# Kernel tuning notes

Measured on AMD Instinct MI355X. Metric: run time of the kernel, lower is better.

The kernel has to match this reference:

```python
import jax, jax.numpy as jnp
import numpy as np

DIM = 768
N_HEADS = 12
HEAD_DIM = DIM // N_HEADS
SCALE = HEAD_DIM ** -0.5


def setup_inputs() -> dict:
    key = jax.random.key(0)
    k_x, k_qkv, k_proj, k_pb = jax.random.split(key, 4)
    B, N = 8, 1024
    x = jax.random.normal(k_x, (B, N, DIM), dtype=jnp.float32)
    # torch nn.Linear weight layout: [out_features, in_features], y = x @ W.T
    w_qkv = jax.random.normal(k_qkv, (3 * DIM, DIM), dtype=jnp.float32) * (DIM ** -0.5)
    w_proj = jax.random.normal(k_proj, (DIM, DIM), dtype=jnp.float32) * (DIM ** -0.5)
    b_proj = jax.random.normal(k_pb, (DIM,), dtype=jnp.float32) * 0.01
    # init_mode='quadratic': alpha=0.125, beta=0.5, gamma=0.0, shape [H,1,1]
    alpha = jnp.full((N_HEADS, 1, 1), 0.125, dtype=jnp.float32)
    beta = jnp.full((N_HEADS, 1, 1), 0.5, dtype=jnp.float32)
    gamma = jnp.zeros((N_HEADS, 1, 1), dtype=jnp.float32)
    return {"x": x, "w_qkv": w_qkv, "w_proj": w_proj, "b_proj": b_proj,
            "alpha": alpha, "beta": beta, "gamma": gamma}


def reference(x, w_qkv, w_proj, b_proj, alpha, beta, gamma):
    B, N, C = x.shape
    qkv = x @ w_qkv.T  # [B, N, 3C]
    qkv = qkv.reshape(B, N, 3, N_HEADS, HEAD_DIM)
    qkv = jnp.transpose(qkv, (2, 0, 3, 1, 4))  # [3, B, H, N, d]
    q, k, v = qkv[0], qkv[1], qkv[2]
    logits = jnp.einsum('bhnd,bhmd->bhnm', q, k) * SCALE  # [B, H, N, N]
    a = alpha[None]  # broadcast over batch: [1, H, 1, 1]
    b = beta[None]
    g = gamma[None]
    attn = jax.nn.relu(a * logits * logits + b * logits + g)
    attn = attn / (jnp.sum(attn, axis=-1, keepdims=True) + 1e-6)
    out = jnp.einsum('bhnm,bhmd->bhnd', attn, v)  # [B, H, N, d]
    out = jnp.transpose(out, (0, 2, 1, 3)).reshape(B, N, C)
    return out @ w_proj.T + b_proj
```

## Files before the change

kernel.cpp:

```cpp
#include <hip/hip_runtime.h>


typedef _Float16 f16x8 __attribute__((ext_vector_type(8)));
typedef _Float16 f16x4 __attribute__((ext_vector_type(4)));
typedef float f32x4 __attribute__((ext_vector_type(4)));

#define NB 8
#define NN 1024
#define NC 768
#define NH 12
#define ND 64
#define TC 2304
#define NM 8192

__device__ __forceinline__ void async16(const void* g, void* l) {
    __builtin_amdgcn_global_load_lds(
        (const __attribute__((address_space(1))) void*)g,
        (__attribute__((address_space(3))) void*)l, 16, 0, 0);
}

__global__ void cvt_f32_f16(const float* __restrict__ s, _Float16* __restrict__ d, int n4) {
    int i = blockIdx.x * 256 + threadIdx.x;
    if (i < n4) {
        float4 v = ((const float4*)s)[i];
        f16x4 o;
        o[0] = (_Float16)v.x; o[1] = (_Float16)v.y;
        o[2] = (_Float16)v.z; o[3] = (_Float16)v.w;
        ((f16x4*)d)[i] = o;
    }
}

__global__ void cvt_split_f32(const float* __restrict__ s, _Float16* __restrict__ hi,
                              _Float16* __restrict__ lo, int n4) {
    int i = blockIdx.x * 256 + threadIdx.x;
    if (i < n4) {
        float4 v = ((const float4*)s)[i];
        f16x4 h, l;
        h[0] = (_Float16)v.x; l[0] = (_Float16)(v.x - (float)h[0]);
        h[1] = (_Float16)v.y; l[1] = (_Float16)(v.y - (float)h[1]);
        h[2] = (_Float16)v.z; l[2] = (_Float16)(v.z - (float)h[2]);
        h[3] = (_Float16)v.w; l[3] = (_Float16)(v.w - (float)h[3]);
        ((f16x4*)hi)[i] = h;
        ((f16x4*)lo)[i] = l;
    }
}

__global__ __launch_bounds__(256) void gemm_qkv(
    const _Float16* __restrict__ Ah, const _Float16* __restrict__ Bh,
    _Float16* __restrict__ q16, _Float16* __restrict__ k16,
    _Float16* __restrict__ vt16)
{
    __shared__ __align__(16) _Float16 sAh[128 * 32];
    __shared__ __align__(16) _Float16 sBh[128 * 32];
    const int tid = threadIdx.x;
    const int lane = tid & 63, wv = tid >> 6;
    const int quad = lane >> 4, l16 = lane & 15;
    const int wm = (wv >> 1) * 64, wn = (wv & 1) * 64;
    const int m0 = blockIdx.x * 128, n0 = blockIdx.y * 128;

    f32x4 acc[4][4] = {};

    for (int k0 = 0; k0 < NC; k0 += 32) {
#pragma unroll
        for (int i = 0; i < 2; i++) {
            int c = tid + i * 256;
            int r = c >> 2, kc = c & 3;
            async16(Ah + (size_t)(m0 + r) * NC + k0 + kc * 8, sAh + c * 8);
            async16(Bh + (size_t)(n0 + r) * NC + k0 + kc * 8, sBh + c * 8);
        }
        __syncthreads();
        f16x8 ah[4], bh[4];
#pragma unroll
        for (int t = 0; t < 4; t++) {
            ah[t] = *(const f16x8*)(sAh + (wm + t * 16 + l16) * 32 + quad * 8);
            bh[t] = *(const f16x8*)(sBh + (wn + t * 16 + l16) * 32 + quad * 8);
        }
#pragma unroll
        for (int i = 0; i < 4; i++)
#pragma unroll
            for (int j = 0; j < 4; j++)
                acc[i][j] = __builtin_amdgcn_mfma_f32_16x16x32_f16(ah[i], bh[j], acc[i][j], 0, 0, 0);
        __syncthreads();
    }

    const int col = n0 + wn + l16;
#pragma unroll
    for (int j = 0; j < 4; j++) {
        int cj = col + j * 16;
        int which = cj / NC;
        int w2 = cj - which * NC;
        int h = w2 >> 6, dd = w2 & 63;
#pragma unroll
        for (int i = 0; i < 4; i++) {
            int row = m0 + wm + i * 16 + quad * 4;
            int b = row >> 10, nr = row & 1023;
            int bhd = b * NH + h;
            if (which == 2) {
                f16x4 v4;
                v4[0] = (_Float16)acc[i][j][0];
                v4[1] = (_Float16)acc[i][j][1];
                v4[2] = (_Float16)acc[i][j][2];
                v4[3] = (_Float16)acc[i][j][3];
                *(f16x4*)(vt16 + ((size_t)(bhd * ND + dd)) * NN + nr) = v4;
            } else {
                _Float16* dst = (which == 0 ? q16 : k16);
#pragma unroll
                for (int r = 0; r < 4; r++)
                    dst[((size_t)(bhd * NN + nr + r)) * ND + dd] = (_Float16)acc[i][j][r];
            }
        }
    }
}

__global__ __launch_bounds__(256) void attn_kernel(
    const _Float16* __restrict__ q16, const _Float16* __restrict__ k16,
    const _Float16* __restrict__ vt16, float* __restrict__ outh32,
    const float* __restrict__ alpha, const float* __restrict__ beta,
    const float* __restrict__ gamma)
{
    const int qt = blockIdx.x, bh = blockIdx.y;
    const int b = bh / NH, h = bh - b * NH;
    const int tid = threadIdx.x, lane = tid & 63, wv = tid >> 6;
    const int quad = lane >> 4, l16 = lane & 15;
    const float a2 = alpha[h] * 0.015625f;
    const float b1 = beta[h] * 0.125f;
    const float g0 = gamma[h];

    __shared__ __align__(16) _Float16 sKh[128 * 64];
    __shared__ __align__(16) _Float16 sVt[64 * 128];

    const _Float16* Qb = q16 + ((size_t)(bh * NN + qt * 128)) * ND;
    const _Float16* Kb = k16 + (size_t)bh * NN * ND;
    const _Float16* Vb = vt16 + (size_t)bh * ND * NN;

    f16x8 qf[2][2];
#pragma unroll
    for (int mt = 0; mt < 2; mt++)
#pragma unroll
        for (int ksd = 0; ksd < 2; ksd++)
            qf[mt][ksd] = *(const f16x8*)(Qb + (size_t)(wv * 32 + mt * 16 + l16) * ND
                                          + ksd * 32 + quad * 8);

    f32x4 O[4][2] = {};
    float dsum[2] = {0.f, 0.f};

    for (int kt = 0; kt < 8; kt++) {
#pragma unroll
        for (int i = 0; i < 4; i++) {
            int P = tid + i * 256;
            int f = P >> 6, q = (P >> 4) & 3, a = (P >> 2) & 3, bb = P & 3;
            int ks2 = f >> 2, T = (f >> 1) & 1, ksd = f & 1;
            int row = ks2 * 32 + 8 * a + 4 * T + bb;
            async16(Kb + (size_t)(kt * 128 + row) * ND + (ksd * 4 + q) * 8, sKh + P * 8);
        }
#pragma unroll
        for (int i = 0; i < 4; i++) {
            int P = tid + i * 256;
            int f = P >> 6, q = (P >> 4) & 3, l = P & 15;
            int ks2 = f >> 2, dt = f & 3;
            async16(Vb + (size_t)(dt * 16 + l) * NN + kt * 128 + (ks2 * 4 + q) * 8,
                    sVt + P * 8);
        }
        __syncthreads();

        f16x8 bfrag[2][4];
#pragma unroll
        for (int T = 0; T < 2; T++) {
            f32x4 S[2][4] = {};
#pragma unroll
            for (int ks2 = 0; ks2 < 4; ks2++) {
#pragma unroll
                for (int ksd = 0; ksd < 2; ksd++) {
                    int addr = (((ks2 * 4 + T * 2 + ksd) * 64) + quad * 16 + l16) * 8;
                    f16x8 ah = *(const f16x8*)(sKh + addr);
#pragma unroll
                    for (int mt = 0; mt < 2; mt++)
                        S[mt][ks2] = __builtin_amdgcn_mfma_f32_16x16x32_f16(ah, qf[mt][ksd], S[mt][ks2], 0, 0, 0);
                }
            }
#pragma unroll
            for (int mt = 0; mt < 2; mt++) {
#pragma unroll
                for (int ks2 = 0; ks2 < 4; ks2++) {
#pragma unroll
                    for (int r = 0; r < 4; r++) {
                        float s = S[mt][ks2][r];
                        float w = fmaxf(fmaf(fmaf(a2, s, b1), s, g0), 0.f);
                        _Float16 wh = (_Float16)w;
                        dsum[mt] += (float)wh;
                        bfrag[mt][ks2][(T << 2) | r] = wh;
                    }
                }
            }
        }

#pragma unroll
        for (int ks2 = 0; ks2 < 4; ks2++) {
#pragma unroll
            for (int dt = 0; dt < 4; dt++) {
                int addr = (((ks2 * 4 + dt) * 64) + quad * 16 + l16) * 8;
                f16x8 vf = *(const f16x8*)(sVt + addr);
#pragma unroll
                for (int mt = 0; mt < 2; mt++)
                    O[dt][mt] = __builtin_amdgcn_mfma_f32_16x16x32_f16(vf, bfrag[mt][ks2], O[dt][mt], 0, 0, 0);
            }
        }
        __syncthreads();
    }

    float rinv[2];
#pragma unroll
    for (int mt = 0; mt < 2; mt++) {
        float v = dsum[mt];
        v += __shfl_xor(v, 16);
        v += __shfl_xor(v, 32);
        rinv[mt] = 1.0f / (v + 1e-6f);
    }

    const int base_row = qt * 128 + wv * 32;
#pragma unroll
    for (int dt = 0; dt < 4; dt++) {
#pragma unroll
        for (int mt = 0; mt < 2; mt++) {
            float4 o4;
            o4.x = O[dt][mt][0] * rinv[mt];
            o4.y = O[dt][mt][1] * rinv[mt];
            o4.z = O[dt][mt][2] * rinv[mt];
            o4.w = O[dt][mt][3] * rinv[mt];
            int row = base_row + mt * 16 + l16;
            int col = h * ND + dt * 16 + quad * 4;
            *(float4*)(outh32 + (size_t)(b * NN + row) * NC + col) = o4;
        }
    }
}

__global__ __launch_bounds__(256) void gemm_proj(
    const float* __restrict__ A,
    const _Float16* __restrict__ Bh, const _Float16* __restrict__ Bl,
    const float* __restrict__ bias, float* __restrict__ out)
{
    __shared__ __align__(16) _Float16 sAh[128 * 32];
    __shared__ __align__(16) _Float16 sAl[128 * 32];
    __shared__ __align__(16) _Float16 sBh[64 * 32];
    __shared__ __align__(16) _Float16 sBl[64 * 32];
    const int tid = threadIdx.x;
    const int lane = tid & 63, wv = tid >> 6;
    const int quad = lane >> 4, l16 = lane & 15;
    const int wm = (wv >> 1) * 64, wn = (wv & 1) * 32;
    const int m0 = blockIdx.x * 128, n0 = blockIdx.y * 64;

    f32x4 acc[4][2] = {};

    for (int k0 = 0; k0 < NC; k0 += 32) {
#pragma unroll
        for (int i = 0; i < 2; i++) {
            int c = tid + i * 256;
            int r = c >> 2, kc = c & 3;
            const float4* pa = (const float4*)(A + (size_t)(m0 + r) * NC + k0 + kc * 8);
            float4 v0 = pa[0], v1 = pa[1];
            f16x8 hi8, lo8;
            hi8[0] = (_Float16)v0.x; lo8[0] = (_Float16)(v0.x - (float)hi8[0]);
            hi8[1] = (_Float16)v0.y; lo8[1] = (_Float16)(v0.y - (float)hi8[1]);
            hi8[2] = (_Float16)v0.z; lo8[2] = (_Float16)(v0.z - (float)hi8[2]);
            hi8[3] = (_Float16)v0.w; lo8[3] = (_Float16)(v0.w - (float)hi8[3]);
            hi8[4] = (_Float16)v1.x; lo8[4] = (_Float16)(v1.x - (float)hi8[4]);
            hi8[5] = (_Float16)v1.y; lo8[5] = (_Float16)(v1.y - (float)hi8[5]);
            hi8[6] = (_Float16)v1.z; lo8[6] = (_Float16)(v1.z - (float)hi8[6]);
            hi8[7] = (_Float16)v1.w; lo8[7] = (_Float16)(v1.w - (float)hi8[7]);
            *(f16x8*)(sAh + c * 8) = hi8;
            *(f16x8*)(sAl + c * 8) = lo8;
        }
        {
            int r = tid >> 2, kc = tid & 3;
            size_t goB = (size_t)(n0 + r) * NC + k0 + kc * 8;
            async16(Bh + goB, sBh + tid * 8);
            async16(Bl + goB, sBl + tid * 8);
        }
        __syncthreads();
        f16x8 ah[4], al[4], bh[2], bl[2];
#pragma unroll
        for (int t = 0; t < 4; t++) {
            ah[t] = *(const f16x8*)(sAh + (wm + t * 16 + l16) * 32 + quad * 8);
            al[t] = *(const f16x8*)(sAl + (wm + t * 16 + l16) * 32 + quad * 8);
        }
#pragma unroll
        for (int t = 0; t < 2; t++) {
            bh[t] = *(const f16x8*)(sBh + (wn + t * 16 + l16) * 32 + quad * 8);
            bl[t] = *(const f16x8*)(sBl + (wn + t * 16 + l16) * 32 + quad * 8);
        }
#pragma unroll
        for (int i = 0; i < 4; i++)
#pragma unroll
            for (int j = 0; j < 2; j++)
                acc[i][j] = __builtin_amdgcn_mfma_f32_16x16x32_f16(ah[i], bh[j], acc[i][j], 0, 0, 0);
#pragma unroll
        for (int i = 0; i < 4; i++)
#pragma unroll
            for (int j = 0; j < 2; j++)
                acc[i][j] = __builtin_amdgcn_mfma_f32_16x16x32_f16(al[i], bh[j], acc[i][j], 0, 0, 0);
#pragma unroll
        for (int i = 0; i < 4; i++)
#pragma unroll
            for (int j = 0; j < 2; j++)
                acc[i][j] = __builtin_amdgcn_mfma_f32_16x16x32_f16(ah[i], bl[j], acc[i][j], 0, 0, 0);
        __syncthreads();
    }

#pragma unroll
    for (int i = 0; i < 4; i++) {
#pragma unroll
        for (int j = 0; j < 2; j++) {
#pragma unroll
            for (int r = 0; r < 4; r++) {
                int row = m0 + wm + i * 16 + quad * 4 + r;
                int col = n0 + wn + j * 16 + l16;
                out[(size_t)row * NC + col] = acc[i][j][r] + bias[col];
            }
        }
    }
}

extern "C" void kernel_launch(void* const* d_in, const int* in_sizes, int n_in,
                              void* d_out, int out_size, void* d_ws, size_t ws_size,
                              hipStream_t stream) {
    const float* x      = (const float*)d_in[0];
    const float* w_qkv  = (const float*)d_in[1];
    const float* w_proj = (const float*)d_in[2];
    const float* b_proj = (const float*)d_in[3];
    const float* alpha  = (const float*)d_in[4];
    const float* beta   = (const float*)d_in[5];
    const float* gamma  = (const float*)d_in[6];
    float* out = (float*)d_out;

    char* ws = (char*)d_ws;
    float*    outh32 = (float*)(ws + 0);
    _Float16* xh     = (_Float16*)(ws + 25165824);
    _Float16* wqkvh  = (_Float16*)(ws + 37748736);
    _Float16* wprojh = (_Float16*)(ws + 41287680);
    _Float16* wprojl = (_Float16*)(ws + 42467328);
    _Float16* q16    = (_Float16*)(ws + 43646976);
    _Float16* k16    = (_Float16*)(ws + 56229888);
    _Float16* vt16   = (_Float16*)(ws + 68812800);

    cvt_f32_f16<<<6144, 256, 0, stream>>>(x, xh, 1572864);
    cvt_f32_f16<<<1728, 256, 0, stream>>>(w_qkv, wqkvh, 442368);
    cvt_split_f32<<<576, 256, 0, stream>>>(w_proj, wprojh, wprojl, 147456);

    gemm_qkv<<<dim3(64, 18), 256, 0, stream>>>(xh, wqkvh, q16, k16, vt16);
    attn_kernel<<<dim3(8, 96), 256, 0, stream>>>(q16, k16, vt16, outh32, alpha, beta, gamma);
    gemm_proj<<<dim3(64, 12), 256, 0, stream>>>(outh32, wprojh, wprojl, b_proj, out);
}
```

Measured before the change: 215.6 us.

## Widen GEMM K-tiles, swizzle LDS layout, stage epilogue stores, pre-split attention output

Both GEMMs now load 64-wide K tiles into a fragment-ordered LDS layout, so each lane's MFMA operand reads are contiguous and conflict-free. Each tile therefore needs half as many barrier round trips. The QKV epilogue stages results through shared memory and writes Q/K rows and V-transpose rows with 16-byte vector stores instead of scattered scalar stores. The attention kernel now writes its output as fp16 hi/lo pairs, so gemm_proj can load A asynchronously instead of converting fp32 in the load loop. The cost is more LDS per block, which may lower occupancy.

```diff
diff --git a/kernel.cpp b/kernel.cpp
--- a/kernel.cpp
+++ b/kernel.cpp
@@ -46,75 +46,99 @@
 }
 
 __global__ __launch_bounds__(256) void gemm_qkv(
-    const _Float16* __restrict__ Ah, const _Float16* __restrict__ Bh,
+    const _Float16* __restrict__ Ah, const _Float16* __restrict__ Bw,
     _Float16* __restrict__ q16, _Float16* __restrict__ k16,
     _Float16* __restrict__ vt16)
 {
-    __shared__ __align__(16) _Float16 sAh[128 * 32];
-    __shared__ __align__(16) _Float16 sBh[128 * 32];
+    __shared__ __align__(16) _Float16 sm[2 * 128 * 64];
+    _Float16* sA = sm;
+    _Float16* sB = sm + 128 * 64;
     const int tid = threadIdx.x;
     const int lane = tid & 63, wv = tid >> 6;
     const int quad = lane >> 4, l16 = lane & 15;
-    const int wm = (wv >> 1) * 64, wn = (wv & 1) * 64;
+    const int wmh = wv >> 1, wnh = wv & 1;
+    const int wm = wmh * 64, wn = wnh * 64;
     const int m0 = blockIdx.x * 128, n0 = blockIdx.y * 128;
 
     f32x4 acc[4][4] = {};
 
-    for (int k0 = 0; k0 < NC; k0 += 32) {
-#pragma unroll
-        for (int i = 0; i < 2; i++) {
-            int c = tid + i * 256;
-            int r = c >> 2, kc = c & 3;
-            async16(Ah + (size_t)(m0 + r) * NC + k0 + kc * 8, sAh + c * 8);
-            async16(Bh + (size_t)(n0 + r) * NC + k0 + kc * 8, sBh + c * 8);
-        }
-        __syncthreads();
-        f16x8 ah[4], bh[4];
-#pragma unroll
-        for (int t = 0; t < 4; t++) {
-            ah[t] = *(const f16x8*)(sAh + (wm + t * 16 + l16) * 32 + quad * 8);
-            bh[t] = *(const f16x8*)(sBh + (wn + t * 16 + l16) * 32 + quad * 8);
-        }
+    for (int k0 = 0; k0 < NC; k0 += 64) {
+#pragma unroll
+        for (int i = 0; i < 4; i++) {
+            int P = tid + i * 256;
+            int f = P >> 6, q = (P >> 4) & 3, l = P & 15;
+            int half = f >> 3, t = (f >> 1) & 3, ksd = f & 1;
+            int row = half * 64 + t * 16 + l;
+            int ch = ksd * 4 + q;
+            async16(Ah + (size_t)(m0 + row) * NC + k0 + ch * 8, sA + P * 8);
+            async16(Bw + (size_t)(n0 + row) * NC + k0 + ch * 8, sB + P * 8);
+        }
+        __syncthreads();
+#pragma unroll
+        for (int ksd = 0; ksd < 2; ksd++) {
+            f16x8 a4[4], b4[4];
+#pragma unroll
+            for (int t = 0; t < 4; t++) {
+                a4[t] = *(const f16x8*)(sA + (((wmh * 4 + t) * 2 + ksd) * 64 + quad * 16 + l16) * 8);
+                b4[t] = *(const f16x8*)(sB + (((wnh * 4 + t) * 2 + ksd) * 64 + quad * 16 + l16) * 8);
+            }
+#pragma unroll
+            for (int i = 0; i < 4; i++)
+#pragma unroll
+                for (int j = 0; j < 4; j++)
+                    acc[i][j] = __builtin_amdgcn_mfma_f32_16x16x32_f16(a4[i], b4[j], acc[i][j], 0, 0, 0);
+        }
+        __syncthreads();
+    }
+
+    _Float16* sT = sm;
+    const bool is_v = (n0 >= 2 * NC);
+    if (!is_v) {
 #pragma unroll
         for (int i = 0; i < 4; i++)
 #pragma unroll
             for (int j = 0; j < 4; j++)
-                acc[i][j] = __builtin_amdgcn_mfma_f32_16x16x32_f16(ah[i], bh[j], acc[i][j], 0, 0, 0);
-        __syncthreads();
-    }
-
-    const int col = n0 + wn + l16;
-#pragma unroll
-    for (int j = 0; j < 4; j++) {
-        int cj = col + j * 16;
-        int which = cj / NC;
-        int w2 = cj - which * NC;
-        int h = w2 >> 6, dd = w2 & 63;
-#pragma unroll
-        for (int i = 0; i < 4; i++) {
-            int row = m0 + wm + i * 16 + quad * 4;
-            int b = row >> 10, nr = row & 1023;
-            int bhd = b * NH + h;
-            if (which == 2) {
+#pragma unroll
+                for (int r = 0; r < 4; r++)
+                    sT[(wm + i * 16 + quad * 4 + r) * 128 + wn + j * 16 + l16] =
+                        (_Float16)acc[i][j][r];
+        __syncthreads();
+        int row = tid >> 1, hh = tid & 1;
+        int grow = m0 + row, b = grow >> 10, nr = grow & 1023;
+        int gc = n0 + hh * 64;
+        int which = gc / NC, w2 = gc - which * NC, h = w2 >> 6;
+        _Float16* dst = which ? k16 : q16;
+        size_t base = ((size_t)((b * NH + h) * NN + nr)) * ND;
+#pragma unroll
+        for (int c = 0; c < 8; c++)
+            *(f16x8*)(dst + base + c * 8) = *(const f16x8*)(sT + row * 128 + hh * 64 + c * 8);
+    } else {
+#pragma unroll
+        for (int i = 0; i < 4; i++)
+#pragma unroll
+            for (int j = 0; j < 4; j++) {
                 f16x4 v4;
                 v4[0] = (_Float16)acc[i][j][0];
                 v4[1] = (_Float16)acc[i][j][1];
                 v4[2] = (_Float16)acc[i][j][2];
                 v4[3] = (_Float16)acc[i][j][3];
-                *(f16x4*)(vt16 + ((size_t)(bhd * ND + dd)) * NN + nr) = v4;
-            } else {
-                _Float16* dst = (which == 0 ? q16 : k16);
-#pragma unroll
-                for (int r = 0; r < 4; r++)
-                    dst[((size_t)(bhd * NN + nr + r)) * ND + dd] = (_Float16)acc[i][j][r];
-            }
-        }
+                *(f16x4*)(sT + (wn + j * 16 + l16) * 128 + wm + i * 16 + quad * 4) = v4;
+            }
+        __syncthreads();
+        int ch = tid >> 1, th = tid & 1;
+        int w2 = n0 - 2 * NC + ch, h = w2 >> 6, dd = w2 & 63;
+        int b = m0 >> 10, nr0 = (m0 & 1023) + th * 64;
+        size_t base = ((size_t)((b * NH + h) * ND + dd)) * NN + nr0;
+#pragma unroll
+        for (int c = 0; c < 8; c++)
+            *(f16x8*)(vt16 + base + c * 8) = *(const f16x8*)(sT + ch * 128 + th * 64 + c * 8);
     }
 }
 
 __global__ __launch_bounds__(256) void attn_kernel(
     const _Float16* __restrict__ q16, const _Float16* __restrict__ k16,
-    const _Float16* __restrict__ vt16, float* __restrict__ outh32,
+    const _Float16* __restrict__ vt16,
+    _Float16* __restrict__ ohA, _Float16* __restrict__ olA,
     const float* __restrict__ alpha, const float* __restrict__ beta,
     const float* __restrict__ gamma)
 {
@@ -222,87 +246,96 @@
     for (int dt = 0; dt < 4; dt++) {
 #pragma unroll
         for (int mt = 0; mt < 2; mt++) {
-            float4 o4;
-            o4.x = O[dt][mt][0] * rinv[mt];
-            o4.y = O[dt][mt][1] * rinv[mt];
-            o4.z = O[dt][mt][2] * rinv[mt];
-            o4.w = O[dt][mt][3] * rinv[mt];
+            f16x4 h4, l4;
+#pragma unroll
+            for (int r = 0; r < 4; r++) {
+                float v = O[dt][mt][r] * rinv[mt];
+                _Float16 hv = (_Float16)v;
+                h4[r] = hv;
+                l4[r] = (_Float16)(v - (float)hv);
+            }
             int row = base_row + mt * 16 + l16;
             int col = h * ND + dt * 16 + quad * 4;
-            *(float4*)(outh32 + (size_t)(b * NN + row) * NC + col) = o4;
+            size_t addr = (size_t)(b * NN + row) * NC + col;
+            *(f16x4*)(ohA + addr) = h4;
+            *(f16x4*)(olA + addr) = l4;
         }
     }
 }
 
 __global__ __launch_bounds__(256) void gemm_proj(
-    const float* __restrict__ A,
+    const _Float16* __restrict__ Ah, const _Float16* __restrict__ Al,
     const _Float16* __restrict__ Bh, const _Float16* __restrict__ Bl,
     const float* __restrict__ bias, float* __restrict__ out)
 {
-    __shared__ __align__(16) _Float16 sAh[128 * 32];
-    __shared__ __align__(16) _Float16 sAl[128 * 32];
-    __shared__ __align__(16) _Float16 sBh[64 * 32];
-    __shared__ __align__(16) _Float16 sBl[64 * 32];
+    __shared__ __align__(16) _Float16 sAh[128 * 64];
+    __shared__ __align__(16) _Float16 sAl[128 * 64];
+    __shared__ __align__(16) _Float16 sBh[64 * 64];
+    __shared__ __align__(16) _Float16 sBl[64 * 64];
     const int tid = threadIdx.x;
     const int lane = tid & 63, wv = tid >> 6;
     const int quad = lane >> 4, l16 = lane & 15;
-    const int wm = (wv >> 1) * 64, wn = (wv & 1) * 32;
+    const int wmh = wv >> 1, wnh = wv & 1;
+    const int wm = wmh * 64, wn = wnh * 32;
     const int m0 = blockIdx.x * 128, n0 = blockIdx.y * 64;
 
     f32x4 acc[4][2] = {};
 
-    for (int k0 = 0; k0 < NC; k0 += 32) {
+    for (int k0 = 0; k0 < NC; k0 += 64) {
+#pragma unroll
+        for (int i = 0; i < 4; i++) {
+            int P = tid + i * 256;
+            int f = P >> 6, q = (P >> 4) & 3, l = P & 15;
+            int half = f >> 3, t = (f >> 1) & 3, ksd = f & 1;
+            int row = half * 64 + t * 16 + l;
+            int ch = ksd * 4 + q;
+            size_t src = (size_t)(m0 + row) * NC + k0 + ch * 8;
+            async16(Ah + src, sAh + P * 8);
+            async16(Al + src, sAl + P * 8);
+        }
 #pragma unroll
         for (int i = 0; i < 2; i++) {
-            int c = tid + i * 256;
-            int r = c >> 2, kc = c & 3;
-            const float4* pa = (const float4*)(A + (size_t)(m0 + r) * NC + k0 + kc * 8);
-            float4 v0 = pa[0], v1 = pa[1];
-            f16x8 hi8, lo8;
-            hi8[0] = (_Float16)v0.x; lo8[0] = (_Float16)(v0.x - (float)hi8[0]);
-            hi8[1] = (_Float16)v0.y; lo8[1] = (_Float16)(v0.y - (float)hi8[1]);
-            hi8[2] = (_Float16)v0.z; lo8[2] = (_Float16)(v0.z - (float)hi8[2]);
-            hi8[3] = (_Float16)v0.w; lo8[3] = (_Float16)(v0.w - (float)hi8[3]);
-            hi8[4] = (_Float16)v1.x; lo8[4] = (_Float16)(v1.x - (float)hi8[4]);
-            hi8[5] = (_Float16)v1.y; lo8[5] = (_Float16)(v1.y - (float)hi8[5]);
-            hi8[6] = (_Float16)v1.z; lo8[6] = (_Float16)(v1.z - (float)hi8[6]);
-            hi8[7] = (_Float16)v1.w; lo8[7] = (_Float16)(v1.w - (float)hi8[7]);
-            *(f16x8*)(sAh + c * 8) = hi8;
-            *(f16x8*)(sAl + c * 8) = lo8;
-        }
-        {
-            int r = tid >> 2, kc = tid & 3;
-            size_t goB = (size_t)(n0 + r) * NC + k0 + kc * 8;
-            async16(Bh + goB, sBh + tid * 8);
-            async16(Bl + goB, sBl + tid * 8);
-        }
-        __syncthreads();
-        f16x8 ah[4], al[4], bh[2], bl[2];
-#pragma unroll
-        for (int t = 0; t < 4; t++) {
-            ah[t] = *(const f16x8*)(sAh + (wm + t * 16 + l16) * 32 + quad * 8);
-            al[t] = *(const f16x8*)(sAl + (wm + t * 16 + l16) * 32 + quad * 8);
-        }
-#pragma unroll
-        for (int t = 0; t < 2; t++) {
-            bh[t] = *(const f16x8*)(sBh + (wn + t * 16 + l16) * 32 + quad * 8);
-            bl[t] = *(const f16x8*)(sBl + (wn + t * 16 + l16) * 32 + quad * 8);
-        }
-#pragma unroll
-        for (int i = 0; i < 4; i++)
-#pragma unroll
-            for (int j = 0; j < 2; j++)
-                acc[i][j] = __builtin_amdgcn_mfma_f32_16x16x32_f16(ah[i], bh[j], acc[i][j], 0, 0, 0);
-#pragma unroll
-        for (int i = 0; i < 4; i++)
-#pragma unroll
-            for (int j = 0; j < 2; j++)
-                acc[i][j] = __builtin_amdgcn_mfma_f32_16x16x32_f16(al[i], bh[j], acc[i][j], 0, 0, 0);
-#pragma unroll
-        for (int i = 0; i < 4; i++)
-#pragma unroll
-            for (int j = 0; j < 2; j++)
-                acc[i][j] = __builtin_amdgcn_mfma_f32_16x16x32_f16(ah[i], bl[j], acc[i][j], 0, 0, 0);
+            int P = tid + i * 256;
+            int f = P >> 6, q = (P >> 4) & 3, l = P & 15;
+            int nh = f >> 2, t = (f >> 1) & 1, ksd = f & 1;
+            int row = nh * 32 + t * 16 + l;
+            int ch = ksd * 4 + q;
+            size_t src = (size_t)(n0 + row) * NC + k0 + ch * 8;
+            async16(Bh + src, sBh + P * 8);
+            async16(Bl + src, sBl + P * 8);
+        }
+        __syncthreads();
+#pragma unroll
+        for (int ksd = 0; ksd < 2; ksd++) {
+            f16x8 a4[4], a4l[4], b4[2], b4l[2];
+#pragma unroll
+            for (int t = 0; t < 4; t++) {
+                int addr = (((wmh * 4 + t) * 2 + ksd) * 64 + quad * 16 + l16) * 8;
+                a4[t]  = *(const f16x8*)(sAh + addr);
+                a4l[t] = *(const f16x8*)(sAl + addr);
+            }
+#pragma unroll
+            for (int t = 0; t < 2; t++) {
+                int addr = (((wnh * 2 + t) * 2 + ksd) * 64 + quad * 16 + l16) * 8;
+                b4[t]  = *(const f16x8*)(sBh + addr);
+                b4l[t] = *(const f16x8*)(sBl + addr);
+            }
+#pragma unroll
+            for (int i = 0; i < 4; i++)
+#pragma unroll
+                for (int j = 0; j < 2; j++)
+                    acc[i][j] = __builtin_amdgcn_mfma_f32_16x16x32_f16(a4[i], b4[j], acc[i][j], 0, 0, 0);
+#pragma unroll
+            for (int i = 0; i < 4; i++)
+#pragma unroll
+                for (int j = 0; j < 2; j++)
+                    acc[i][j] = __builtin_amdgcn_mfma_f32_16x16x32_f16(a4l[i], b4[j], acc[i][j], 0, 0, 0);
+#pragma unroll
+            for (int i = 0; i < 4; i++)
+#pragma unroll
+                for (int j = 0; j < 2; j++)
+                    acc[i][j] = __builtin_amdgcn_mfma_f32_16x16x32_f16(a4[i], b4l[j], acc[i][j], 0, 0, 0);
+        }
         __syncthreads();
     }
 
@@ -333,7 +366,8 @@
     float* out = (float*)d_out;
 
     char* ws = (char*)d_ws;
-    float*    outh32 = (float*)(ws + 0);
+    _Float16* ohA    = (_Float16*)(ws + 0);
+    _Float16* olA    = (_Float16*)(ws + 12582912);
     _Float16* xh     = (_Float16*)(ws + 25165824);
     _Float16* wqkvh  = (_Float16*)(ws + 37748736);
     _Float16* wprojh = (_Float16*)(ws + 41287680);
@@ -347,6 +381,6 @@
     cvt_split_f32<<<576, 256, 0, stream>>>(w_proj, wprojh, wprojl, 147456);
 
     gemm_qkv<<<dim3(64, 18), 256, 0, stream>>>(xh, wqkvh, q16, k16, vt16);
-    attn_kernel<<<dim3(8, 96), 256, 0, stream>>>(q16, k16, vt16, outh32, alpha, beta, gamma);
-    gemm_proj<<<dim3(64, 12), 256, 0, stream>>>(outh32, wprojh, wprojl, b_proj, out);
-}
+    attn_kernel<<<dim3(8, 96), 256, 0, stream>>>(q16, k16, vt16, ohA, olA, alpha, beta, gamma);
+    gemm_proj<<<dim3(64, 12), 256, 0, stream>>>(ohA, olA, wprojh, wprojl, b_proj, out);
+}
```

Measured after the change: 274.8 us. 1.27x slower.
